# Performance work log

Measured on AMD Instinct MI355X. Metric: run time of the kernel, lower is better.

Reference implementation:

```python
import jax, jax.numpy as jnp
import numpy as np

SEQ, BATCH, IN_DIM, HID, NQ = 256, 512, 512, 512, 32


def setup_inputs() -> dict:
    key = jax.random.key(0)
    k_in, k_fw, k_fb, k_ow, k_ob = jax.random.split(key, 5)
    s_fc = 1.0 / np.sqrt(IN_DIM + HID)
    s_out = 1.0 / np.sqrt(NQ)
    return {
        "inputs": jax.random.normal(k_in, (SEQ, BATCH, IN_DIM), dtype=jnp.float32),
        "fc_w": jax.random.uniform(k_fw, (NQ, IN_DIM + HID), jnp.float32, -s_fc, s_fc),
        "fc_b": jax.random.uniform(k_fb, (NQ,), jnp.float32, -s_fc, s_fc),
        "out_w": jax.random.uniform(k_ow, (HID, NQ), jnp.float32, -s_out, s_out),
        "out_b": jax.random.uniform(k_ob, (HID,), jnp.float32, -s_out, s_out),
    }


def _quantum_gate(q_in):
    # RX(x_i) on wire i then CNOT ladder; <Z_k> = prod_{j<=k} cos(x_j)
    return jnp.cumprod(jnp.cos(q_in), axis=-1)


def reference(inputs, fc_w, fc_b, out_w, out_b):
    batch = inputs.shape[1]
    h0 = jnp.zeros((batch, HID), dtype=inputs.dtype)
    c0 = jnp.zeros((batch, HID), dtype=inputs.dtype)

    def step(carry, x):
        hx, cx = carry
        combined = jnp.concatenate([x, hx], axis=1)            # [B, IN+HID]
        q_in = combined @ fc_w.T + fc_b                        # [B, NQ]
        q = _quantum_gate(q_in)                                # [B, NQ]
        f = jax.nn.sigmoid(q) @ out_w.T + out_b                # [B, HID]
        i = f                                                  # same circuit & weights as f
        g = jnp.tanh(q) @ out_w.T + out_b
        o = f                                                  # same as f
        cx = f * cx + i * g
        hx = o * jnp.tanh(cx)
        return (hx, cx), hx

    (hx, cx), outputs = jax.lax.scan(step, (h0, c0), inputs)
    return outputs, hx, cx
```

## Files before the change

kernel.cpp:

```cpp
#include <hip/hip_runtime.h>
#include <math.h>

#define SEQ 256
#define BATCH 512
#define IN_DIM 512
#define HID 512
#define NQ 32

typedef float v2f __attribute__((ext_vector_type(2)));

__device__ __forceinline__ float fast_rcp(float x) { return __builtin_amdgcn_rcpf(x); }

__device__ __forceinline__ float tanh_fast(float x) {
    float a = fabsf(x);
    float e = __expf(-2.0f * a);
    float r = (1.0f - e) * fast_rcp(1.0f + e);
    return copysignf(r, x);
}

template <int CTRL>
__device__ __forceinline__ float dpp_add(float x) {
    int t = __builtin_amdgcn_update_dpp(0, __float_as_int(x), CTRL, 0xF, 0xF, false);
    return x + __int_as_float(t);
}
__device__ __forceinline__ float reduce16_add(float x) {
    x = dpp_add<0xB1>(x);
    x = dpp_add<0x4E>(x);
    x = dpp_add<0x141>(x);
    x = dpp_add<0x140>(x);
    return x;
}
__device__ __forceinline__ float reduce4_add(float x) {
    x = dpp_add<0xB1>(x);
    x = dpp_add<0x4E>(x);
    return x;
}
template <int CTRL, int ROW_MASK>
__device__ __forceinline__ float dpp_mul1(float x) {
    int t = __builtin_amdgcn_update_dpp(0x3f800000 , __float_as_int(x),
                                        CTRL, ROW_MASK, 0xF, false);
    return x * __int_as_float(t);
}
__device__ __forceinline__ float scan32_mul(float x) {
    x = dpp_mul1<0x111, 0xF>(x);
    x = dpp_mul1<0x112, 0xF>(x);
    x = dpp_mul1<0x114, 0xF>(x);
    x = dpp_mul1<0x118, 0xF>(x);
    x = dpp_mul1<0x142, 0xA>(x);
    return x;
}

#define BLOCK_BARRIER_LDS() asm volatile("s_waitcnt lgkmcnt(0)\n\ts_barrier" ::: "memory")

__global__ __launch_bounds__(256, 4) void xp_kernel(const float* __restrict__ x,
                                                    const float* __restrict__ fc_w,
                                                    const float* __restrict__ fc_b,
                                                    float* __restrict__ xp) {
    const int tid = threadIdx.x;
    const int g2 = tid >> 4;
    const int s  = tid & 15;

    __shared__ float4 tile4[16 * 128];

    v2f wA_lo[8], wA_hi[8], wB_lo[8], wB_hi[8];
    {
        const float* wrA = fc_w + (size_t)(g2 * 2 + 0) * (IN_DIM + HID) + 4 * s;
        const float* wrB = fc_w + (size_t)(g2 * 2 + 1) * (IN_DIM + HID) + 4 * s;
#pragma unroll
        for (int j = 0; j < 8; ++j) {
            float4 a = *reinterpret_cast<const float4*>(wrA + 64 * j);
            float4 b = *reinterpret_cast<const float4*>(wrB + 64 * j);
            wA_lo[j] = (v2f){a.x, a.y}; wA_hi[j] = (v2f){a.z, a.w};
            wB_lo[j] = (v2f){b.x, b.y}; wB_hi[j] = (v2f){b.z, b.w};
        }
    }
    const float2 bias2 = reinterpret_cast<const float2*>(fc_b)[g2];

    const float4* x4 = reinterpret_cast<const float4*>(x) + (size_t)blockIdx.x * (16 * 128);
#pragma unroll
    for (int q = 0; q < 8; ++q)
        tile4[tid + 256 * q] = x4[tid + 256 * q];
    __syncthreads();

    const int row0 = blockIdx.x * 16;
    float2* xp2 = reinterpret_cast<float2*>(xp);
    for (int rp = 0; rp < 8; ++rp) {
        const int r0 = 2 * rp, r1 = 2 * rp + 1;
        v2f aA0 = (v2f){0.f, 0.f}, aA1 = aA0, aB0 = aA0, aB1 = aA0;
        v2f bA0 = aA0, bA1 = aA0, bB0 = aA0, bB1 = aA0;
#pragma unroll
        for (int j = 0; j < 8; j += 2) {
            float4 h0 = tile4[r0 * 128 + s + 16 * j];
            float4 h1 = tile4[r1 * 128 + s + 16 * j];
            v2f h0lo = (v2f){h0.x, h0.y}, h0hi = (v2f){h0.z, h0.w};
            v2f h1lo = (v2f){h1.x, h1.y}, h1hi = (v2f){h1.z, h1.w};
            aA0 = __builtin_elementwise_fma(h0lo, wA_lo[j], aA0);
            aA0 = __builtin_elementwise_fma(h0hi, wA_hi[j], aA0);
            aA1 = __builtin_elementwise_fma(h0lo, wB_lo[j], aA1);
            aA1 = __builtin_elementwise_fma(h0hi, wB_hi[j], aA1);
            aB0 = __builtin_elementwise_fma(h1lo, wA_lo[j], aB0);
            aB0 = __builtin_elementwise_fma(h1hi, wA_hi[j], aB0);
            aB1 = __builtin_elementwise_fma(h1lo, wB_lo[j], aB1);
            aB1 = __builtin_elementwise_fma(h1hi, wB_hi[j], aB1);
            float4 g0 = tile4[r0 * 128 + s + 16 * (j + 1)];
            float4 g1 = tile4[r1 * 128 + s + 16 * (j + 1)];
            v2f g0lo = (v2f){g0.x, g0.y}, g0hi = (v2f){g0.z, g0.w};
            v2f g1lo = (v2f){g1.x, g1.y}, g1hi = (v2f){g1.z, g1.w};
            bA0 = __builtin_elementwise_fma(g0lo, wA_lo[j + 1], bA0);
            bA0 = __builtin_elementwise_fma(g0hi, wA_hi[j + 1], bA0);
            bA1 = __builtin_elementwise_fma(g0lo, wB_lo[j + 1], bA1);
            bA1 = __builtin_elementwise_fma(g0hi, wB_hi[j + 1], bA1);
            bB0 = __builtin_elementwise_fma(g1lo, wA_lo[j + 1], bB0);
            bB0 = __builtin_elementwise_fma(g1hi, wA_hi[j + 1], bB0);
            bB1 = __builtin_elementwise_fma(g1lo, wB_lo[j + 1], bB1);
            bB1 = __builtin_elementwise_fma(g1hi, wB_hi[j + 1], bB1);
        }
        v2f sA0 = aA0 + bA0, sA1 = aA1 + bA1, sB0 = aB0 + bB0, sB1 = aB1 + bB1;
        float rA0 = reduce16_add(sA0.x + sA0.y);
        float rA1 = reduce16_add(sA1.x + sA1.y);
        float rB0 = reduce16_add(sB0.x + sB0.y);
        float rB1 = reduce16_add(sB1.x + sB1.y);
        if (s == 0) {
            xp2[(size_t)(row0 + r0) * 16 + g2] = make_float2(rA0 + bias2.x, rA1 + bias2.y);
            xp2[(size_t)(row0 + r1) * 16 + g2] = make_float2(rB0 + bias2.x, rB1 + bias2.y);
        }
    }
}

__global__ __launch_bounds__(256)
__attribute__((amdgpu_waves_per_eu(2, 2)))
void rnn_kernel(const float* __restrict__ xp,
                const float* __restrict__ fc_w,
                const float* __restrict__ out_w,
                const float* __restrict__ out_b,
                float* __restrict__ out) {
    const int b = blockIdx.x;
    const int tid = threadIdx.x;
    const int w4 = tid >> 6;
    const int lane = tid & 63;
    const int l31 = lane & 31;
    const int grp = lane >> 2;
    const int sl = lane & 3;

    __shared__ __align__(16) float hbuf[HID];
    __shared__ __align__(16) float pbuf[2][4][NQ];
    __shared__ __align__(16) float pwbuf[4][64];
    __shared__ __align__(16) float xps[SEQ * NQ];

    v2f whA_lo[8], whA_hi[8], whB_lo[8], whB_hi[8];
    {
        const int kbase = IN_DIM + 128 * w4 + 4 * sl;
        const float* wrA = fc_w + (size_t)(grp * 2 + 0) * (IN_DIM + HID) + kbase;
        const float* wrB = fc_w + (size_t)(grp * 2 + 1) * (IN_DIM + HID) + kbase;
#pragma unroll
        for (int j = 0; j < 8; ++j) {
            float4 a = *reinterpret_cast<const float4*>(wrA + 16 * j);
            float4 c = *reinterpret_cast<const float4*>(wrB + 16 * j);
            whA_lo[j] = (v2f){a.x, a.y}; whA_hi[j] = (v2f){a.z, a.w};
            whB_lo[j] = (v2f){c.x, c.y}; whB_hi[j] = (v2f){c.z, c.w};
        }
    }
    const int hid0 = 128 * w4 + lane;
    const int hid1 = hid0 + 64;
    v2f ow0v[16], ow1v[16];
    {
        const float4* o0 = reinterpret_cast<const float4*>(out_w + (size_t)hid0 * NQ);
        const float4* o1 = reinterpret_cast<const float4*>(out_w + (size_t)hid1 * NQ);
#pragma unroll
        for (int q4 = 0; q4 < 8; ++q4) {
            float4 a = o0[q4], bq = o1[q4];
            ow0v[2 * q4 + 0] = (v2f){a.x, a.y};
            ow0v[2 * q4 + 1] = (v2f){a.z, a.w};
            ow1v[2 * q4 + 0] = (v2f){bq.x, bq.y};
            ow1v[2 * q4 + 1] = (v2f){bq.z, bq.w};
        }
    }
    const float ob0 = out_b[hid0];
    const float ob1 = out_b[hid1];

    {
        const float4* xpg = reinterpret_cast<const float4*>(xp);
        float4* xps4 = reinterpret_cast<float4*>(xps);
#pragma unroll
        for (int k = 0; k < 8; ++k) {
            int idx = tid + 256 * k;
            int t = idx >> 3, q4 = idx & 7;
            xps4[idx] = xpg[((size_t)t * BATCH + b) * 8 + q4];
        }
    }
    hbuf[tid] = 0.0f;
    hbuf[tid + 256] = 0.0f;
    float c0 = 0.0f, c1 = 0.0f;
    __syncthreads();

    float* hx_out = out + (size_t)SEQ * BATCH * HID + (size_t)b * HID;
    float* cx_out = hx_out + (size_t)BATCH * HID;

    const float4* h4s = reinterpret_cast<const float4*>(hbuf) + (32 * w4 + sl);

    int par = 0;
    for (int t = 0; t < SEQ; ++t) {
        v2f aA = (v2f){0.f, 0.f}, aB = aA, bA = aA, bB = aA;
#pragma unroll
        for (int j = 0; j < 8; j += 2) {
            float4 hv = h4s[4 * j];
            v2f hlo = (v2f){hv.x, hv.y}, hhi = (v2f){hv.z, hv.w};
            aA = __builtin_elementwise_fma(hlo, whA_lo[j], aA);
            aA = __builtin_elementwise_fma(hhi, whA_hi[j], aA);
            aB = __builtin_elementwise_fma(hlo, whB_lo[j], aB);
            aB = __builtin_elementwise_fma(hhi, whB_hi[j], aB);
            float4 gv = h4s[4 * (j + 1)];
            v2f glo = (v2f){gv.x, gv.y}, ghi = (v2f){gv.z, gv.w};
            bA = __builtin_elementwise_fma(glo, whA_lo[j + 1], bA);
            bA = __builtin_elementwise_fma(ghi, whA_hi[j + 1], bA);
            bB = __builtin_elementwise_fma(glo, whB_lo[j + 1], bB);
            bB = __builtin_elementwise_fma(ghi, whB_hi[j + 1], bB);
        }
        v2f sA = aA + bA, sB = aB + bB;
        float rA = reduce4_add(sA.x + sA.y);
        float rB = reduce4_add(sB.x + sB.y);
        if (sl == 0)
            *reinterpret_cast<float2*>(&pbuf[par][w4][2 * grp]) = make_float2(rA, rB);

        BLOCK_BARRIER_LDS();

        {
            const float* pb = &pbuf[par][0][0];
            float qin = (pb[l31] + pb[32 + l31]) + (pb[64 + l31] + pb[96 + l31])
                      + xps[t * NQ + l31];
            float pp = scan32_mul(__cosf(qin));
            float arg = (lane < 32) ? -pp : (-2.0f * pp);
            float e = __expf(arg);
            float num = (lane < 32) ? 1.0f : (1.0f - e);
            float val = num * fast_rcp(1.0f + e);
            pwbuf[w4][lane] = val;
        }

        const float4* sb4 = reinterpret_cast<const float4*>(&pwbuf[w4][0]);
        const float4* tb4 = sb4 + 8;
        v2f f0a = (v2f){0.f, 0.f}, f0b = f0a, g0a = f0a, g0b = f0a;
        v2f f1a = f0a, f1b = f0a, g1a = f0a, g1b = f0a;
#pragma unroll
        for (int m = 0; m < 8; ++m) {
            float4 sv = sb4[m];
            float4 tv = tb4[m];
            v2f slo = (v2f){sv.x, sv.y}, shi = (v2f){sv.z, sv.w};
            v2f tlo = (v2f){tv.x, tv.y}, thi = (v2f){tv.z, tv.w};
            f0a = __builtin_elementwise_fma(slo, ow0v[2 * m + 0], f0a);
            f0b = __builtin_elementwise_fma(shi, ow0v[2 * m + 1], f0b);
            g0a = __builtin_elementwise_fma(tlo, ow0v[2 * m + 0], g0a);
            g0b = __builtin_elementwise_fma(thi, ow0v[2 * m + 1], g0b);
            f1a = __builtin_elementwise_fma(slo, ow1v[2 * m + 0], f1a);
            f1b = __builtin_elementwise_fma(shi, ow1v[2 * m + 1], f1b);
            g1a = __builtin_elementwise_fma(tlo, ow1v[2 * m + 0], g1a);
            g1b = __builtin_elementwise_fma(thi, ow1v[2 * m + 1], g1b);
        }
        v2f sf0 = f0a + f0b, sg0 = g0a + g0b, sf1 = f1a + f1b, sg1 = g1a + g1b;
        float f0 = ob0 + sf0.x + sf0.y, g0 = ob0 + sg0.x + sg0.y;
        float f1 = ob1 + sf1.x + sf1.y, g1 = ob1 + sg1.x + sg1.y;
        c0 = f0 * (c0 + g0);
        c1 = f1 * (c1 + g1);
        float h0 = f0 * tanh_fast(c0);
        float h1 = f1 * tanh_fast(c1);

        hbuf[hid0] = h0;
        hbuf[hid1] = h1;
        float* orow = out + ((size_t)t * BATCH + b) * HID;
        orow[hid0] = h0;
        orow[hid1] = h1;
        if (t == SEQ - 1) {
            hx_out[hid0] = h0; hx_out[hid1] = h1;
            cx_out[hid0] = c0; cx_out[hid1] = c1;
        }
        par ^= 1;
    }
}

extern "C" void kernel_launch(void* const* d_in, const int* in_sizes, int n_in,
                              void* d_out, int out_size, void* d_ws, size_t ws_size,
                              hipStream_t stream) {
    const float* inputs = (const float*)d_in[0];
    const float* fc_w   = (const float*)d_in[1];
    const float* fc_b   = (const float*)d_in[2];
    const float* out_w  = (const float*)d_in[3];
    const float* out_b  = (const float*)d_in[4];
    float* out = (float*)d_out;
    float* xp  = (float*)d_ws;

    xp_kernel<<<(SEQ * BATCH) / 16, 256, 0, stream>>>(inputs, fc_w, fc_b, xp);
    rnn_kernel<<<BATCH, 256, 0, stream>>>(xp, fc_w, out_w, out_b, out);
}
```

Before: 365.8 us.

## Shrink recurrent block to two waves with four hidden units per thread

The per-batch recurrent kernel now uses 128 threads (2 waves) instead of 256. Each thread holds twice as many hidden-weight registers and computes four hidden units instead of two. This halves the partial-sum reduction across waves and makes each block-wide barrier cheaper. In exchange, per-thread serial work and register pressure go up, and with waves_per_eu set to 1 there is less latency hiding per step.

```diff
diff --git a/kernel.cpp b/kernel.cpp
--- a/kernel.cpp
+++ b/kernel.cpp
@@ -127,8 +127,8 @@
     }
 }
 
-__global__ __launch_bounds__(256)
-__attribute__((amdgpu_waves_per_eu(2, 2)))
+__global__ __launch_bounds__(128)
+__attribute__((amdgpu_waves_per_eu(1, 1)))
 void rnn_kernel(const float* __restrict__ xp,
                 const float* __restrict__ fc_w,
                 const float* __restrict__ out_w,
@@ -136,73 +136,70 @@
                 float* __restrict__ out) {
     const int b = blockIdx.x;
     const int tid = threadIdx.x;
-    const int w4 = tid >> 6;
+    const int w2 = tid >> 6;
     const int lane = tid & 63;
     const int l31 = lane & 31;
     const int grp = lane >> 2;
     const int sl = lane & 3;
 
     __shared__ __align__(16) float hbuf[HID];
-    __shared__ __align__(16) float pbuf[2][4][NQ];
-    __shared__ __align__(16) float pwbuf[4][64];
+    __shared__ __align__(16) float pbuf[2][2][NQ];
+    __shared__ __align__(16) float pwbuf[2][64];
     __shared__ __align__(16) float xps[SEQ * NQ];
 
-    v2f whA_lo[8], whA_hi[8], whB_lo[8], whB_hi[8];
+    v2f whA_lo[16], whA_hi[16], whB_lo[16], whB_hi[16];
     {
-        const int kbase = IN_DIM + 128 * w4 + 4 * sl;
+        const int kbase = IN_DIM + 256 * w2 + 4 * sl;
         const float* wrA = fc_w + (size_t)(grp * 2 + 0) * (IN_DIM + HID) + kbase;
         const float* wrB = fc_w + (size_t)(grp * 2 + 1) * (IN_DIM + HID) + kbase;
 #pragma unroll
-        for (int j = 0; j < 8; ++j) {
+        for (int j = 0; j < 16; ++j) {
             float4 a = *reinterpret_cast<const float4*>(wrA + 16 * j);
             float4 c = *reinterpret_cast<const float4*>(wrB + 16 * j);
             whA_lo[j] = (v2f){a.x, a.y}; whA_hi[j] = (v2f){a.z, a.w};
             whB_lo[j] = (v2f){c.x, c.y}; whB_hi[j] = (v2f){c.z, c.w};
         }
     }
-    const int hid0 = 128 * w4 + lane;
-    const int hid1 = hid0 + 64;
-    v2f ow0v[16], ow1v[16];
-    {
-        const float4* o0 = reinterpret_cast<const float4*>(out_w + (size_t)hid0 * NQ);
-        const float4* o1 = reinterpret_cast<const float4*>(out_w + (size_t)hid1 * NQ);
+    const int hidb = 256 * w2 + lane;
+    v2f owv[4][16];
+    float ob[4];
+#pragma unroll
+    for (int m = 0; m < 4; ++m) {
+        const float4* o = reinterpret_cast<const float4*>(out_w + (size_t)(hidb + 64 * m) * NQ);
 #pragma unroll
         for (int q4 = 0; q4 < 8; ++q4) {
-            float4 a = o0[q4], bq = o1[q4];
-            ow0v[2 * q4 + 0] = (v2f){a.x, a.y};
-            ow0v[2 * q4 + 1] = (v2f){a.z, a.w};
-            ow1v[2 * q4 + 0] = (v2f){bq.x, bq.y};
-            ow1v[2 * q4 + 1] = (v2f){bq.z, bq.w};
-        }
-    }
-    const float ob0 = out_b[hid0];
-    const float ob1 = out_b[hid1];
+            float4 a = o[q4];
+            owv[m][2 * q4 + 0] = (v2f){a.x, a.y};
+            owv[m][2 * q4 + 1] = (v2f){a.z, a.w};
+        }
+        ob[m] = out_b[hidb + 64 * m];
+    }
 
     {
         const float4* xpg = reinterpret_cast<const float4*>(xp);
         float4* xps4 = reinterpret_cast<float4*>(xps);
 #pragma unroll
-        for (int k = 0; k < 8; ++k) {
-            int idx = tid + 256 * k;
+        for (int k = 0; k < 16; ++k) {
+            int idx = tid + 128 * k;
             int t = idx >> 3, q4 = idx & 7;
             xps4[idx] = xpg[((size_t)t * BATCH + b) * 8 + q4];
         }
     }
-    hbuf[tid] = 0.0f;
-    hbuf[tid + 256] = 0.0f;
-    float c0 = 0.0f, c1 = 0.0f;
+#pragma unroll
+    for (int m = 0; m < 4; ++m) hbuf[tid + 128 * m] = 0.0f;
+    float cst[4] = {0.f, 0.f, 0.f, 0.f};
     __syncthreads();
 
     float* hx_out = out + (size_t)SEQ * BATCH * HID + (size_t)b * HID;
     float* cx_out = hx_out + (size_t)BATCH * HID;
 
-    const float4* h4s = reinterpret_cast<const float4*>(hbuf) + (32 * w4 + sl);
+    const float4* h4s = reinterpret_cast<const float4*>(hbuf) + (64 * w2 + sl);
 
     int par = 0;
     for (int t = 0; t < SEQ; ++t) {
         v2f aA = (v2f){0.f, 0.f}, aB = aA, bA = aA, bB = aA;
 #pragma unroll
-        for (int j = 0; j < 8; j += 2) {
+        for (int j = 0; j < 16; j += 2) {
             float4 hv = h4s[4 * j];
             v2f hlo = (v2f){hv.x, hv.y}, hhi = (v2f){hv.z, hv.w};
             aA = __builtin_elementwise_fma(hlo, whA_lo[j], aA);
@@ -220,57 +217,53 @@
         float rA = reduce4_add(sA.x + sA.y);
         float rB = reduce4_add(sB.x + sB.y);
         if (sl == 0)
-            *reinterpret_cast<float2*>(&pbuf[par][w4][2 * grp]) = make_float2(rA, rB);
+            *reinterpret_cast<float2*>(&pbuf[par][w2][2 * grp]) = make_float2(rA, rB);
 
         BLOCK_BARRIER_LDS();
 
         {
-            const float* pb = &pbuf[par][0][0];
-            float qin = (pb[l31] + pb[32 + l31]) + (pb[64 + l31] + pb[96 + l31])
-                      + xps[t * NQ + l31];
+            float qin = pbuf[par][0][l31] + pbuf[par][1][l31] + xps[t * NQ + l31];
             float pp = scan32_mul(__cosf(qin));
             float arg = (lane < 32) ? -pp : (-2.0f * pp);
             float e = __expf(arg);
             float num = (lane < 32) ? 1.0f : (1.0f - e);
             float val = num * fast_rcp(1.0f + e);
-            pwbuf[w4][lane] = val;
-        }
-
-        const float4* sb4 = reinterpret_cast<const float4*>(&pwbuf[w4][0]);
+            pwbuf[w2][lane] = val;
+        }
+
+        const float4* sb4 = reinterpret_cast<const float4*>(&pwbuf[w2][0]);
         const float4* tb4 = sb4 + 8;
-        v2f f0a = (v2f){0.f, 0.f}, f0b = f0a, g0a = f0a, g0b = f0a;
-        v2f f1a = f0a, f1b = f0a, g1a = f0a, g1b = f0a;
-#pragma unroll
-        for (int m = 0; m < 8; ++m) {
-            float4 sv = sb4[m];
-            float4 tv = tb4[m];
+        v2f fa[4], fb[4], ga[4], gb[4];
+#pragma unroll
+        for (int m = 0; m < 4; ++m) { fa[m] = (v2f){0.f, 0.f}; fb[m] = fa[m]; ga[m] = fa[m]; gb[m] = fa[m]; }
+#pragma unroll
+        for (int mm = 0; mm < 8; ++mm) {
+            float4 sv = sb4[mm];
+            float4 tv = tb4[mm];
             v2f slo = (v2f){sv.x, sv.y}, shi = (v2f){sv.z, sv.w};
             v2f tlo = (v2f){tv.x, tv.y}, thi = (v2f){tv.z, tv.w};
-            f0a = __builtin_elementwise_fma(slo, ow0v[2 * m + 0], f0a);
-            f0b = __builtin_elementwise_fma(shi, ow0v[2 * m + 1], f0b);
-            g0a = __builtin_elementwise_fma(tlo, ow0v[2 * m + 0], g0a);
-            g0b = __builtin_elementwise_fma(thi, ow0v[2 * m + 1], g0b);
-            f1a = __builtin_elementwise_fma(slo, ow1v[2 * m + 0], f1a);
-            f1b = __builtin_elementwise_fma(shi, ow1v[2 * m + 1], f1b);
-            g1a = __builtin_elementwise_fma(tlo, ow1v[2 * m + 0], g1a);
-            g1b = __builtin_elementwise_fma(thi, ow1v[2 * m + 1], g1b);
-        }
-        v2f sf0 = f0a + f0b, sg0 = g0a + g0b, sf1 = f1a + f1b, sg1 = g1a + g1b;
-        float f0 = ob0 + sf0.x + sf0.y, g0 = ob0 + sg0.x + sg0.y;
-        float f1 = ob1 + sf1.x + sf1.y, g1 = ob1 + sg1.x + sg1.y;
-        c0 = f0 * (c0 + g0);
-        c1 = f1 * (c1 + g1);
-        float h0 = f0 * tanh_fast(c0);
-        float h1 = f1 * tanh_fast(c1);
-
-        hbuf[hid0] = h0;
-        hbuf[hid1] = h1;
+#pragma unroll
+            for (int m = 0; m < 4; ++m) {
+                fa[m] = __builtin_elementwise_fma(slo, owv[m][2 * mm + 0], fa[m]);
+                fb[m] = __builtin_elementwise_fma(shi, owv[m][2 * mm + 1], fb[m]);
+                ga[m] = __builtin_elementwise_fma(tlo, owv[m][2 * mm + 0], ga[m]);
+                gb[m] = __builtin_elementwise_fma(thi, owv[m][2 * mm + 1], gb[m]);
+            }
+        }
         float* orow = out + ((size_t)t * BATCH + b) * HID;
-        orow[hid0] = h0;
-        orow[hid1] = h1;
-        if (t == SEQ - 1) {
-            hx_out[hid0] = h0; hx_out[hid1] = h1;
-            cx_out[hid0] = c0; cx_out[hid1] = c1;
+#pragma unroll
+        for (int m = 0; m < 4; ++m) {
+            v2f sf = fa[m] + fb[m], sg = ga[m] + gb[m];
+            float f = ob[m] + sf.x + sf.y;
+            float g = ob[m] + sg.x + sg.y;
+            cst[m] = f * (cst[m] + g);
+            float h = f * tanh_fast(cst[m]);
+            hbuf[hidb + 64 * m] = h;
+            orow[hidb + 64 * m] = h;
+            if (t == SEQ - 1) {
+                hx_out[hidb + 64 * m] = h;
+                cx_out[hidb + 64 * m] = cst[m];
+            }
         }
         par ^= 1;
     }
@@ -288,5 +281,5 @@
     float* xp  = (float*)d_ws;
 
     xp_kernel<<<(SEQ * BATCH) / 16, 256, 0, stream>>>(inputs, fc_w, fc_b, xp);
-    rnn_kernel<<<BATCH, 256, 0, stream>>>(xp, fc_w, out_w, out_b, out);
-}
+    rnn_kernel<<<BATCH, 128, 0, stream>>>(xp, fc_w, out_w, out_b, out);
+}
```

After: 468.0 us. 27.9% more time.

## Split recurrent step across 8 waves with one hidden unit per thread

Applied to the files above, without the earlier changes.

Doubles the rnn_kernel block from 256 to 512 threads. Each thread now handles one hidden unit and one quantum row, where before it handled two of each, and the h·W_h partial product uses 2-lane groups over 64-wide K slices instead of 4-lane groups over 128-wide slices. The per-thread serial work and register load per timestep roughly halve, which should shorten the latency-bound recurrence. In exchange the barrier now spans 8 waves, the partial-sum reduction reads 8 slices, and occupancy is pinned at 4 waves per EU.

```diff
diff --git a/kernel.cpp b/kernel.cpp
--- a/kernel.cpp
+++ b/kernel.cpp
@@ -28,11 +28,6 @@
     x = dpp_add<0x4E>(x);
     x = dpp_add<0x141>(x);
     x = dpp_add<0x140>(x);
-    return x;
-}
-__device__ __forceinline__ float reduce4_add(float x) {
-    x = dpp_add<0xB1>(x);
-    x = dpp_add<0x4E>(x);
     return x;
 }
 template <int CTRL, int ROW_MASK>
@@ -127,8 +122,8 @@
     }
 }
 
-__global__ __launch_bounds__(256)
-__attribute__((amdgpu_waves_per_eu(2, 2)))
+__global__ __launch_bounds__(512)
+__attribute__((amdgpu_waves_per_eu(4, 4)))
 void rnn_kernel(const float* __restrict__ xp,
                 const float* __restrict__ fc_w,
                 const float* __restrict__ out_w,
@@ -136,141 +131,114 @@
                 float* __restrict__ out) {
     const int b = blockIdx.x;
     const int tid = threadIdx.x;
-    const int w4 = tid >> 6;
+    const int w8 = tid >> 6;
     const int lane = tid & 63;
     const int l31 = lane & 31;
-    const int grp = lane >> 2;
-    const int sl = lane & 3;
+    const int grp = lane >> 1;
+    const int sl = lane & 1;
 
     __shared__ __align__(16) float hbuf[HID];
-    __shared__ __align__(16) float pbuf[2][4][NQ];
-    __shared__ __align__(16) float pwbuf[4][64];
+    __shared__ __align__(16) float pbuf[2][8][NQ];
+    __shared__ __align__(16) float pwbuf[8][64];
     __shared__ __align__(16) float xps[SEQ * NQ];
 
-    v2f whA_lo[8], whA_hi[8], whB_lo[8], whB_hi[8];
-    {
-        const int kbase = IN_DIM + 128 * w4 + 4 * sl;
-        const float* wrA = fc_w + (size_t)(grp * 2 + 0) * (IN_DIM + HID) + kbase;
-        const float* wrB = fc_w + (size_t)(grp * 2 + 1) * (IN_DIM + HID) + kbase;
+    v2f wh_lo[8], wh_hi[8];
+    {
+        const float* wr = fc_w + (size_t)grp * (IN_DIM + HID) + IN_DIM + 64 * w8 + 4 * sl;
 #pragma unroll
         for (int j = 0; j < 8; ++j) {
-            float4 a = *reinterpret_cast<const float4*>(wrA + 16 * j);
-            float4 c = *reinterpret_cast<const float4*>(wrB + 16 * j);
-            whA_lo[j] = (v2f){a.x, a.y}; whA_hi[j] = (v2f){a.z, a.w};
-            whB_lo[j] = (v2f){c.x, c.y}; whB_hi[j] = (v2f){c.z, c.w};
-        }
-    }
-    const int hid0 = 128 * w4 + lane;
-    const int hid1 = hid0 + 64;
-    v2f ow0v[16], ow1v[16];
-    {
-        const float4* o0 = reinterpret_cast<const float4*>(out_w + (size_t)hid0 * NQ);
-        const float4* o1 = reinterpret_cast<const float4*>(out_w + (size_t)hid1 * NQ);
+            float4 a = *reinterpret_cast<const float4*>(wr + 8 * j);
+            wh_lo[j] = (v2f){a.x, a.y}; wh_hi[j] = (v2f){a.z, a.w};
+        }
+    }
+    const int hid = 64 * w8 + lane;
+    v2f owv[16];
+    {
+        const float4* o = reinterpret_cast<const float4*>(out_w + (size_t)hid * NQ);
 #pragma unroll
         for (int q4 = 0; q4 < 8; ++q4) {
-            float4 a = o0[q4], bq = o1[q4];
-            ow0v[2 * q4 + 0] = (v2f){a.x, a.y};
-            ow0v[2 * q4 + 1] = (v2f){a.z, a.w};
-            ow1v[2 * q4 + 0] = (v2f){bq.x, bq.y};
-            ow1v[2 * q4 + 1] = (v2f){bq.z, bq.w};
-        }
-    }
-    const float ob0 = out_b[hid0];
-    const float ob1 = out_b[hid1];
+            float4 a = o[q4];
+            owv[2 * q4 + 0] = (v2f){a.x, a.y};
+            owv[2 * q4 + 1] = (v2f){a.z, a.w};
+        }
+    }
+    const float ob = out_b[hid];
 
     {
         const float4* xpg = reinterpret_cast<const float4*>(xp);
         float4* xps4 = reinterpret_cast<float4*>(xps);
 #pragma unroll
-        for (int k = 0; k < 8; ++k) {
-            int idx = tid + 256 * k;
+        for (int k = 0; k < 4; ++k) {
+            int idx = tid + 512 * k;
             int t = idx >> 3, q4 = idx & 7;
             xps4[idx] = xpg[((size_t)t * BATCH + b) * 8 + q4];
         }
     }
     hbuf[tid] = 0.0f;
-    hbuf[tid + 256] = 0.0f;
-    float c0 = 0.0f, c1 = 0.0f;
+    float c = 0.0f;
     __syncthreads();
 
     float* hx_out = out + (size_t)SEQ * BATCH * HID + (size_t)b * HID;
     float* cx_out = hx_out + (size_t)BATCH * HID;
 
-    const float4* h4s = reinterpret_cast<const float4*>(hbuf) + (32 * w4 + sl);
+    const float4* h4s = reinterpret_cast<const float4*>(hbuf) + (16 * w8 + sl);
 
     int par = 0;
     for (int t = 0; t < SEQ; ++t) {
-        v2f aA = (v2f){0.f, 0.f}, aB = aA, bA = aA, bB = aA;
+        v2f aA = (v2f){0.f, 0.f}, bA = aA;
 #pragma unroll
         for (int j = 0; j < 8; j += 2) {
-            float4 hv = h4s[4 * j];
-            v2f hlo = (v2f){hv.x, hv.y}, hhi = (v2f){hv.z, hv.w};
-            aA = __builtin_elementwise_fma(hlo, whA_lo[j], aA);
-            aA = __builtin_elementwise_fma(hhi, whA_hi[j], aA);
-            aB = __builtin_elementwise_fma(hlo, whB_lo[j], aB);
-            aB = __builtin_elementwise_fma(hhi, whB_hi[j], aB);
-            float4 gv = h4s[4 * (j + 1)];
-            v2f glo = (v2f){gv.x, gv.y}, ghi = (v2f){gv.z, gv.w};
-            bA = __builtin_elementwise_fma(glo, whA_lo[j + 1], bA);
-            bA = __builtin_elementwise_fma(ghi, whA_hi[j + 1], bA);
-            bB = __builtin_elementwise_fma(glo, whB_lo[j + 1], bB);
-            bB = __builtin_elementwise_fma(ghi, whB_hi[j + 1], bB);
-        }
-        v2f sA = aA + bA, sB = aB + bB;
-        float rA = reduce4_add(sA.x + sA.y);
-        float rB = reduce4_add(sB.x + sB.y);
-        if (sl == 0)
-            *reinterpret_cast<float2*>(&pbuf[par][w4][2 * grp]) = make_float2(rA, rB);
+            float4 hv = h4s[2 * j];
+            aA = __builtin_elementwise_fma((v2f){hv.x, hv.y}, wh_lo[j], aA);
+            aA = __builtin_elementwise_fma((v2f){hv.z, hv.w}, wh_hi[j], aA);
+            float4 gv = h4s[2 * (j + 1)];
+            bA = __builtin_elementwise_fma((v2f){gv.x, gv.y}, wh_lo[j + 1], bA);
+            bA = __builtin_elementwise_fma((v2f){gv.z, gv.w}, wh_hi[j + 1], bA);
+        }
+        v2f sA = aA + bA;
+        float r = dpp_add<0xB1>(sA.x + sA.y);
+        if (sl == 0) pbuf[par][w8][grp] = r;
 
         BLOCK_BARRIER_LDS();
 
         {
             const float* pb = &pbuf[par][0][0];
-            float qin = (pb[l31] + pb[32 + l31]) + (pb[64 + l31] + pb[96 + l31])
-                      + xps[t * NQ + l31];
+            float q01 = pb[l31] + pb[32 + l31];
+            float q23 = pb[64 + l31] + pb[96 + l31];
+            float q45 = pb[128 + l31] + pb[160 + l31];
+            float q67 = pb[192 + l31] + pb[224 + l31];
+            float qin = ((q01 + q23) + (q45 + q67)) + xps[t * NQ + l31];
             float pp = scan32_mul(__cosf(qin));
             float arg = (lane < 32) ? -pp : (-2.0f * pp);
             float e = __expf(arg);
             float num = (lane < 32) ? 1.0f : (1.0f - e);
             float val = num * fast_rcp(1.0f + e);
-            pwbuf[w4][lane] = val;
-        }
-
-        const float4* sb4 = reinterpret_cast<const float4*>(&pwbuf[w4][0]);
+            pwbuf[w8][lane] = val;
+        }
+
+        const float4* sb4 = reinterpret_cast<const float4*>(&pwbuf[w8][0]);
         const float4* tb4 = sb4 + 8;
-        v2f f0a = (v2f){0.f, 0.f}, f0b = f0a, g0a = f0a, g0b = f0a;
-        v2f f1a = f0a, f1b = f0a, g1a = f0a, g1b = f0a;
+        v2f fa = (v2f){0.f, 0.f}, fb = fa, ga = fa, gb = fa;
 #pragma unroll
         for (int m = 0; m < 8; ++m) {
             float4 sv = sb4[m];
             float4 tv = tb4[m];
-            v2f slo = (v2f){sv.x, sv.y}, shi = (v2f){sv.z, sv.w};
-            v2f tlo = (v2f){tv.x, tv.y}, thi = (v2f){tv.z, tv.w};
-            f0a = __builtin_elementwise_fma(slo, ow0v[2 * m + 0], f0a);
-            f0b = __builtin_elementwise_fma(shi, ow0v[2 * m + 1], f0b);
-            g0a = __builtin_elementwise_fma(tlo, ow0v[2 * m + 0], g0a);
-            g0b = __builtin_elementwise_fma(thi, ow0v[2 * m + 1], g0b);
-            f1a = __builtin_elementwise_fma(slo, ow1v[2 * m + 0], f1a);
-            f1b = __builtin_elementwise_fma(shi, ow1v[2 * m + 1], f1b);
-            g1a = __builtin_elementwise_fma(tlo, ow1v[2 * m + 0], g1a);
-            g1b = __builtin_elementwise_fma(thi, ow1v[2 * m + 1], g1b);
-        }
-        v2f sf0 = f0a + f0b, sg0 = g0a + g0b, sf1 = f1a + f1b, sg1 = g1a + g1b;
-        float f0 = ob0 + sf0.x + sf0.y, g0 = ob0 + sg0.x + sg0.y;
-        float f1 = ob1 + sf1.x + sf1.y, g1 = ob1 + sg1.x + sg1.y;
-        c0 = f0 * (c0 + g0);
-        c1 = f1 * (c1 + g1);
-        float h0 = f0 * tanh_fast(c0);
-        float h1 = f1 * tanh_fast(c1);
-
-        hbuf[hid0] = h0;
-        hbuf[hid1] = h1;
-        float* orow = out + ((size_t)t * BATCH + b) * HID;
-        orow[hid0] = h0;
-        orow[hid1] = h1;
+            fa = __builtin_elementwise_fma((v2f){sv.x, sv.y}, owv[2 * m + 0], fa);
+            fb = __builtin_elementwise_fma((v2f){sv.z, sv.w}, owv[2 * m + 1], fb);
+            ga = __builtin_elementwise_fma((v2f){tv.x, tv.y}, owv[2 * m + 0], ga);
+            gb = __builtin_elementwise_fma((v2f){tv.z, tv.w}, owv[2 * m + 1], gb);
+        }
+        v2f sf = fa + fb, sg = ga + gb;
+        float f = ob + sf.x + sf.y;
+        float g = ob + sg.x + sg.y;
+        c = f * (c + g);
+        float h = f * tanh_fast(c);
+
+        hbuf[hid] = h;
+        out[((size_t)t * BATCH + b) * HID + hid] = h;
         if (t == SEQ - 1) {
-            hx_out[hid0] = h0; hx_out[hid1] = h1;
-            cx_out[hid0] = c0; cx_out[hid1] = c1;
+            hx_out[hid] = h;
+            cx_out[hid] = c;
         }
         par ^= 1;
     }
@@ -288,5 +256,5 @@
     float* xp  = (float*)d_ws;
 
     xp_kernel<<<(SEQ * BATCH) / 16, 256, 0, stream>>>(inputs, fc_w, fc_b, xp);
-    rnn_kernel<<<BATCH, 256, 0, stream>>>(xp, fc_w, out_w, out_b, out);
-}
+    rnn_kernel<<<BATCH, 512, 0, stream>>>(xp, fc_w, out_w, out_b, out);
+}
```

Measured after the change: 408.5 us. 11.7% more time.
